# Kernel tuning notes

Hardware: AMD Instinct MI355X
Metric: run time of the kernel (lower is better)

The kernel has to match this reference:

```python
import jax, jax.numpy as jnp
import numpy as np
from jax import lax

BEV_SIZE = 250
BEV_RANGE = 50.0
BEV_RES = 0.4
SZ = BEV_SIZE * BEV_SIZE
N_POINTS = 5_000_000
EPS = 1e-5


def setup_inputs() -> dict:
    key = jax.random.key(0)
    ks = jax.random.split(key, 8)
    # points: x,y in [-55,55) (some out of range), z in [-3,5), intensity in [0,1)
    xy = jax.random.uniform(ks[0], (N_POINTS, 2), jnp.float32, -55.0, 55.0)
    z = jax.random.uniform(ks[1], (N_POINTS, 1), jnp.float32, -3.0, 5.0)
    it = jax.random.uniform(ks[2], (N_POINTS, 1), jnp.float32, 0.0, 1.0)
    points = jnp.concatenate([xy, z, it], axis=1)

    def he(k, shape):
        fan_in = shape[1] * shape[2] * shape[3]
        return jax.random.normal(k, shape, jnp.float32) * np.sqrt(2.0 / fan_in)

    return {
        "points": points,
        "w1": he(ks[3], (32, 4, 3, 3)), "b1": jnp.zeros(32), "g1": jnp.ones(32), "beta1": jnp.zeros(32),
        "w2": he(ks[4], (64, 32, 3, 3)), "b2": jnp.zeros(64), "g2": jnp.ones(64), "beta2": jnp.zeros(64),
        "w3": he(ks[5], (64, 64, 3, 3)), "b3": jnp.zeros(64), "g3": jnp.ones(64), "beta3": jnp.zeros(64),
    }


def points_to_bev(points):
    x, y, z, inten = points[:, 0], points[:, 1], points[:, 2], points[:, 3]
    valid = (x >= -BEV_RANGE) & (x < BEV_RANGE) & (y >= -BEV_RANGE) & (y < BEV_RANGE)
    xi = jnp.clip(((x + BEV_RANGE) / BEV_RES).astype(jnp.int32), 0, BEV_SIZE - 1)
    yi = jnp.clip(((y + BEV_RANGE) / BEV_RES).astype(jnp.int32), 0, BEV_SIZE - 1)
    # invalid points routed to an extra dummy bin SZ, sliced off afterwards
    flat = jnp.where(valid, yi * BEV_SIZE + xi, SZ)

    max_z = jnp.full(SZ + 1, -jnp.inf, jnp.float32).at[flat].max(z)[:SZ]
    max_z = jnp.where(jnp.isinf(max_z), 0.0, max_z)
    min_z = jnp.full(SZ + 1, jnp.inf, jnp.float32).at[flat].min(z)[:SZ]
    min_z = jnp.where(jnp.isinf(min_z), 0.0, min_z)
    density = jnp.zeros(SZ + 1, jnp.float32).at[flat].add(1.0)[:SZ]
    isum = jnp.zeros(SZ + 1, jnp.float32).at[flat].add(inten)[:SZ]
    mean_i = jnp.where(density > 0, isum / jnp.maximum(density, 1.0), 0.0)

    bev = jnp.stack([max_z, min_z, jnp.log1p(density), mean_i], axis=0)
    return bev.reshape(4, BEV_SIZE, BEV_SIZE)


def conv_bn_relu(x, w, b, g, beta):
    # x: (1, Cin, H, W), w: (Cout, Cin, 3, 3)
    y = lax.conv_general_dilated(x, w, (1, 1), "SAME",
                                 dimension_numbers=("NCHW", "OIHW", "NCHW"))
    y = y + b[None, :, None, None]
    # BatchNorm2d in training mode: batch stats over (N, H, W)
    mu = jnp.mean(y, axis=(0, 2, 3), keepdims=True)
    var = jnp.mean((y - mu) ** 2, axis=(0, 2, 3), keepdims=True)
    y = (y - mu) * lax.rsqrt(var + EPS)
    y = y * g[None, :, None, None] + beta[None, :, None, None]
    return jax.nn.relu(y)


def reference(points, w1, b1, g1, beta1, w2, b2, g2, beta2, w3, b3, g3, beta3):
    bev = points_to_bev(points)[None]  # (1, 4, 250, 250)
    h = conv_bn_relu(bev, w1, b1, g1, beta1)
    h = conv_bn_relu(h, w2, b2, g2, beta2)
    h = conv_bn_relu(h, w3, b3, g3, beta3)
    return h  # (1, 64, 250, 250)
```

## Files before the change

### kernel.cpp

```cpp
#include <hip/hip_runtime.h>


constexpr int BEVW = 250;
constexpr int SZC  = BEVW * BEVW;
constexpr int NB   = 512;
constexpr int PPT  = 16;
constexpr int CHUNK = 256 * PPT;
constexpr int NBKT = 100;
constexpr int NCELL = 625;
constexpr int CAPB = 43008;
constexpr int NSL  = 8;

__device__ __forceinline__ unsigned f2ord(float f) {
    unsigned u = __float_as_uint(f);
    return (u & 0x80000000u) ? ~u : (u | 0x80000000u);
}
__device__ __forceinline__ float ord2f(unsigned u) {
    unsigned b = (u & 0x80000000u) ? (u & 0x7FFFFFFFu) : ~u;
    return __uint_as_float(b);
}

__global__ void k_initg(unsigned* __restrict__ gcnt) {
    if (threadIdx.x < 128) gcnt[threadIdx.x] = 0u;
}

__launch_bounds__(256)
__global__ void k_bucket(const float4* __restrict__ pts, int n,
                         unsigned long long* __restrict__ recs,
                         unsigned* __restrict__ gcnt) {
    __shared__ unsigned lcnt[NBKT];
    __shared__ unsigned lbase[NBKT];
    const int tid = threadIdx.x;
    if (tid < NBKT) lcnt[tid] = 0u;
    __syncthreads();

    const int ppb = (n + NB - 1) / NB;
    const int start = blockIdx.x * ppb;
    const int end = min(start + ppb, n);

    for (int c0 = start; c0 < end; c0 += CHUNK) {
        unsigned long long rec[PPT];
        int bkt[PPT];
        unsigned slot[PPT];
        unsigned vmask = 0u;
#pragma unroll
        for (int k = 0; k < PPT; ++k) {
            int p = c0 + k * 256 + tid;
            if (p >= end) continue;
            float4 q = pts[p];
            if (!(q.x >= -50.0f && q.x < 50.0f && q.y >= -50.0f && q.y < 50.0f))
                continue;
            int xi = (int)((q.x + 50.0f) / 0.4f);
            int yi = (int)((q.y + 50.0f) / 0.4f);
            xi = min(max(xi, 0), BEVW - 1);
            yi = min(max(yi, 0), BEVW - 1);
            int b  = (yi / 25) * 10 + (xi / 25);
            int cl = (yi % 25) * 25 + (xi % 25);
            unsigned iq = (unsigned)(q.w * 4194304.0f);
            rec[k] = ((unsigned long long)f2ord(q.z) << 32) |
                     ((unsigned long long)(unsigned)cl << 22) | iq;
            bkt[k] = b;
            slot[k] = atomicAdd(&lcnt[b], 1u);
            vmask |= 1u << k;
        }
        __syncthreads();
        if (tid < NBKT) {
            unsigned c = lcnt[tid];
            if (c) lbase[tid] = atomicAdd(&gcnt[tid], c);
            lcnt[tid] = 0u;
        }
        __syncthreads();
#pragma unroll
        for (int k = 0; k < PPT; ++k) {
            if (!((vmask >> k) & 1u)) continue;
            unsigned idx = lbase[bkt[k]] + slot[k];
            if (idx < (unsigned)CAPB)
                recs[(size_t)bkt[k] * CAPB + idx] = rec[k];
        }
    }
}

__launch_bounds__(1024)
__global__ void k_reduce(const unsigned long long* __restrict__ recs,
                         const unsigned* __restrict__ gcnt,
                         float* __restrict__ bev) {
    __shared__ unsigned mxA[NCELL], mnA[NCELL], ctA[NCELL], siA[NCELL];
    const int b = blockIdx.x;
    for (int i = threadIdx.x; i < NCELL; i += 1024) {
        mxA[i] = 0u; mnA[i] = 0xFFFFFFFFu; ctA[i] = 0u; siA[i] = 0u;
    }
    __syncthreads();
    const unsigned nb = min(gcnt[b], (unsigned)CAPB);
    const unsigned long long* rb = recs + (size_t)b * CAPB;
    for (unsigned i = threadIdx.x; i < nb; i += 1024) {
        unsigned long long r = rb[i];
        unsigned zo = (unsigned)(r >> 32);
        unsigned cl = ((unsigned)(r >> 22)) & 0x3FFu;
        unsigned iq = (unsigned)r & 0x3FFFFFu;
        atomicMax(&mxA[cl], zo);
        atomicMin(&mnA[cl], zo);
        atomicAdd(&ctA[cl], 1u);
        atomicAdd(&siA[cl], iq);
    }
    __syncthreads();
    const int tx = b % 10, ty = b / 10;
    for (int i = threadIdx.x; i < NCELL; i += 1024) {
        int cy = ty * 25 + i / 25, cx = tx * 25 + i % 25;
        int cell = cy * BEVW + cx;
        unsigned c = ctA[i];
        bool has = c > 0u;
        float dn = (float)c;
        float isum = (float)siA[i] * (1.0f / 4194304.0f);
        bev[0 * SZC + cell] = has ? ord2f(mxA[i]) : 0.0f;
        bev[1 * SZC + cell] = has ? ord2f(mnA[i]) : 0.0f;
        bev[2 * SZC + cell] = log1pf(dn);
        bev[3 * SZC + cell] = has ? isum / dn : 0.0f;
    }
}

__global__ void k_wt(const float* __restrict__ w, float* __restrict__ wt,
                     int CIN, int COUT) {
    int i = blockIdx.x * blockDim.x + threadIdx.x;
    if (i >= COUT * CIN * 9) return;
    int oc = i / (CIN * 9);
    int r  = i % (CIN * 9);
    int ic = r / 9, k = r % 9;
    wt[(ic * 9 + k) * COUT + oc] = w[i];
}

template <int CIN, int COUT, int ICB, int OCG>
__launch_bounds__(256)
__global__ void k_conv3x3(const float* __restrict__ in, const float* __restrict__ wt,
                          const float* __restrict__ bias, float* __restrict__ out) {
    __shared__ float s_in[ICB][18][18];

    const int tid = threadIdx.x;
    const int px = tid & 15, py = tid >> 4;
    const int tile = blockIdx.x;
    const int tx = (tile & 15) * 16, ty = (tile >> 4) * 16;
    const int oc0 = blockIdx.y * OCG;

    float acc[OCG];
#pragma unroll
    for (int o = 0; o < OCG; ++o) acc[o] = 0.0f;

    for (int ic0 = 0; ic0 < CIN; ic0 += ICB) {
        __syncthreads();
        for (int e = tid; e < ICB * 18 * 18; e += 256) {
            int c = e / 324, r = (e % 324) / 18, q = e % 18;
            int gy = ty - 1 + r, gx = tx - 1 + q;
            float v = 0.0f;
            if (gy >= 0 && gy < BEVW && gx >= 0 && gx < BEVW)
                v = in[(ic0 + c) * SZC + gy * BEVW + gx];
            s_in[c][r][q] = v;
        }
        __syncthreads();

        for (int icl = 0; icl < ICB; ++icl) {
#pragma unroll
            for (int k = 0; k < 9; ++k) {
                float v = s_in[icl][py + k / 3][px + k % 3];
                const float* wk = wt + ((size_t)((ic0 + icl) * 9 + k) * COUT + oc0);
#pragma unroll
                for (int j = 0; j < OCG; ++j)
                    acc[j] = fmaf(v, wk[j], acc[j]);
            }
        }
    }

    int ox = tx + px, oy = ty + py;
    if (ox < BEVW && oy < BEVW) {
#pragma unroll
        for (int o = 0; o < OCG; ++o)
            out[(oc0 + o) * SZC + oy * BEVW + ox] = acc[o] + bias[oc0 + o];
    }
}

__global__ void k_bnstats1(const float* __restrict__ y, double* __restrict__ part) {
    const int c = blockIdx.x, s = blockIdx.y;
    const int lo = s * ((SZC + NSL - 1) / NSL);
    const int hi = min(lo + (SZC + NSL - 1) / NSL, SZC);
    const float* p = y + (size_t)c * SZC;
    double sm = 0.0, s2 = 0.0;
    for (int i = lo + threadIdx.x; i < hi; i += 256) {
        float v = p[i];
        sm += (double)v;
        s2 += (double)v * (double)v;
    }
    for (int off = 32; off; off >>= 1) {
        sm += __shfl_down(sm, off);
        s2 += __shfl_down(s2, off);
    }
    __shared__ double sh[8];
    int wid = threadIdx.x >> 6;
    if ((threadIdx.x & 63) == 0) { sh[wid * 2] = sm; sh[wid * 2 + 1] = s2; }
    __syncthreads();
    if (threadIdx.x == 0) {
        double S = 0.0, S2 = 0.0;
        for (int wv = 0; wv < 4; ++wv) { S += sh[wv * 2]; S2 += sh[wv * 2 + 1]; }
        part[(c * NSL + s) * 2]     = S;
        part[(c * NSL + s) * 2 + 1] = S2;
    }
}

__global__ void k_bnstats2(const double* __restrict__ part, float* __restrict__ stats) {
    int c = threadIdx.x;
    double S = 0.0, S2 = 0.0;
    for (int s = 0; s < NSL; ++s) {
        S  += part[(c * NSL + s) * 2];
        S2 += part[(c * NSL + s) * 2 + 1];
    }
    double mu  = S / (double)SZC;
    double var = S2 / (double)SZC - mu * mu;
    stats[c * 2]     = (float)mu;
    stats[c * 2 + 1] = (float)(1.0 / sqrt(var + 1e-5));
}

__global__ void k_bnrelu(const float* __restrict__ y, const float* __restrict__ stats,
                         const float* __restrict__ g, const float* __restrict__ beta,
                         float* __restrict__ out) {
    int c = blockIdx.y;
    int i = blockIdx.x * blockDim.x + threadIdx.x;
    if (i >= SZC) return;
    float mu = stats[c * 2], rs = stats[c * 2 + 1];
    size_t idx = (size_t)c * SZC + i;
    float v = (y[idx] - mu) * rs * g[c] + beta[c];
    out[idx] = v > 0.0f ? v : 0.0f;
}

extern "C" void kernel_launch(void* const* d_in, const int* in_sizes, int n_in,
                              void* d_out, int out_size, void* d_ws, size_t ws_size,
                              hipStream_t stream) {
    const float4* pts = (const float4*)d_in[0];
    const float* w1 = (const float*)d_in[1];
    const float* b1 = (const float*)d_in[2];
    const float* g1 = (const float*)d_in[3];
    const float* be1 = (const float*)d_in[4];
    const float* w2 = (const float*)d_in[5];
    const float* b2 = (const float*)d_in[6];
    const float* g2 = (const float*)d_in[7];
    const float* be2 = (const float*)d_in[8];
    const float* w3 = (const float*)d_in[9];
    const float* b3 = (const float*)d_in[10];
    const float* g3 = (const float*)d_in[11];
    const float* be3 = (const float*)d_in[12];

    float* ws = (float*)d_ws;
    unsigned long long* recs = (unsigned long long*)ws;
    constexpr size_t RECS_F = (size_t)NBKT * CAPB * 2;
    unsigned* gcnt = (unsigned*)(ws + RECS_F);
    float* bev = ws + RECS_F + 128;
    float* st1 = bev + 4 * SZC;
    float* st2 = st1 + 64;
    float* st3 = st2 + 128;
    double* bnpart = (double*)(st3 + 128);
    float* wt1 = (float*)(bnpart + 64 * NSL * 2);
    float* wt2 = wt1 + 32 * 4 * 9;
    float* wt3 = wt2 + 64 * 32 * 9;
    float* y1  = ws;
    float* y2  = ws + 2000000;
    float* out = (float*)d_out;

    int n = in_sizes[0] / 4;

    const int cellBlocks = (SZC + 255) / 256;

    k_wt<<<(32 * 4 * 9 + 255) / 256, 256, 0, stream>>>(w1, wt1, 4, 32);
    k_wt<<<(64 * 32 * 9 + 255) / 256, 256, 0, stream>>>(w2, wt2, 32, 64);
    k_wt<<<(64 * 64 * 9 + 255) / 256, 256, 0, stream>>>(w3, wt3, 64, 64);

    k_initg<<<1, 128, 0, stream>>>(gcnt);
    k_bucket<<<NB, 256, 0, stream>>>(pts, n, recs, gcnt);
    k_reduce<<<NBKT, 1024, 0, stream>>>(recs, gcnt, bev);

    k_conv3x3<4, 32, 4, 16><<<dim3(256, 2), 256, 0, stream>>>(bev, wt1, b1, y1);
    k_bnstats1<<<dim3(32, NSL), 256, 0, stream>>>(y1, bnpart);
    k_bnstats2<<<1, 32, 0, stream>>>(bnpart, st1);
    k_bnrelu<<<dim3(cellBlocks, 32), 256, 0, stream>>>(y1, st1, g1, be1, y1);

    k_conv3x3<32, 64, 8, 16><<<dim3(256, 4), 256, 0, stream>>>(y1, wt2, b2, y2);
    k_bnstats1<<<dim3(64, NSL), 256, 0, stream>>>(y2, bnpart);
    k_bnstats2<<<1, 64, 0, stream>>>(bnpart, st2);
    k_bnrelu<<<dim3(cellBlocks, 64), 256, 0, stream>>>(y2, st2, g2, be2, y2);

    k_conv3x3<64, 64, 8, 16><<<dim3(256, 4), 256, 0, stream>>>(y2, wt3, b3, out);
    k_bnstats1<<<dim3(64, NSL), 256, 0, stream>>>(out, bnpart);
    k_bnstats2<<<1, 64, 0, stream>>>(bnpart, st3);
    k_bnrelu<<<dim3(cellBlocks, 64), 256, 0, stream>>>(out, st3, g3, be3, out);
}
```

Measured before the change: 289.0 us.

## Fold BN+ReLU into next conv's input load and split-K conv over channels

The BatchNorm+ReLU of layers 1 and 2 is now applied while the next convolution loads its input tile, which removes two standalone elementwise passes over the activations. When the workspace is large enough, conv2 and conv3 split the input channels into two halves along grid z and write two partial outputs. Later kernels (stats, next conv, final BN+ReLU) sum those partials on read. The split doubles the grid to fill more CUs, at the cost of extra partial-buffer traffic and recomputing the BN affine in every halo load. The workspace layout moves to the tail of the buffer, and whether the split is used depends on ws_size.

```diff
diff --git a/kernel.cpp b/kernel.cpp
--- a/kernel.cpp
+++ b/kernel.cpp
@@ -128,10 +128,13 @@
     wt[(ic * 9 + k) * COUT + oc] = w[i];
 }
 
-template <int CIN, int COUT, int ICB, int OCG>
+template <int CINH, int COUT, int ICB, int OCG, bool FUSE_BN, bool SUM2, bool SPLIT>
 __launch_bounds__(256)
-__global__ void k_conv3x3(const float* __restrict__ in, const float* __restrict__ wt,
-                          const float* __restrict__ bias, float* __restrict__ out) {
+__global__ void k_conv(const float* __restrict__ ina, const float* __restrict__ inb,
+                       const float* __restrict__ wt, const float* __restrict__ bias,
+                       const float* __restrict__ stats, const float* __restrict__ g,
+                       const float* __restrict__ beta,
+                       float* __restrict__ outa, float* __restrict__ outb) {
     __shared__ float s_in[ICB][18][18];
 
     const int tid = threadIdx.x;
@@ -139,28 +142,40 @@
     const int tile = blockIdx.x;
     const int tx = (tile & 15) * 16, ty = (tile >> 4) * 16;
     const int oc0 = blockIdx.y * OCG;
+    const int z = SPLIT ? blockIdx.z : 0;
+    const int icB = z * CINH;
+    float* out = (SPLIT && z) ? outb : outa;
 
     float acc[OCG];
 #pragma unroll
     for (int o = 0; o < OCG; ++o) acc[o] = 0.0f;
 
-    for (int ic0 = 0; ic0 < CIN; ic0 += ICB) {
+    for (int ic0 = 0; ic0 < CINH; ic0 += ICB) {
         __syncthreads();
         for (int e = tid; e < ICB * 18 * 18; e += 256) {
             int c = e / 324, r = (e % 324) / 18, q = e % 18;
+            int cg = icB + ic0 + c;
             int gy = ty - 1 + r, gx = tx - 1 + q;
             float v = 0.0f;
-            if (gy >= 0 && gy < BEVW && gx >= 0 && gx < BEVW)
-                v = in[(ic0 + c) * SZC + gy * BEVW + gx];
+            if (gy >= 0 && gy < BEVW && gx >= 0 && gx < BEVW) {
+                size_t idx = (size_t)cg * SZC + gy * BEVW + gx;
+                v = ina[idx];
+                if (SUM2) v += inb[idx];
+                if (FUSE_BN) {
+                    float t = (v - stats[2 * cg]) * stats[2 * cg + 1] * g[cg] + beta[cg];
+                    v = t > 0.0f ? t : 0.0f;
+                }
+            }
             s_in[c][r][q] = v;
         }
         __syncthreads();
 
+#pragma unroll 2
         for (int icl = 0; icl < ICB; ++icl) {
 #pragma unroll
             for (int k = 0; k < 9; ++k) {
                 float v = s_in[icl][py + k / 3][px + k % 3];
-                const float* wk = wt + ((size_t)((ic0 + icl) * 9 + k) * COUT + oc0);
+                const float* wk = wt + ((size_t)((icB + ic0 + icl) * 9 + k) * COUT + oc0);
 #pragma unroll
                 for (int j = 0; j < OCG; ++j)
                     acc[j] = fmaf(v, wk[j], acc[j]);
@@ -170,20 +185,24 @@
 
     int ox = tx + px, oy = ty + py;
     if (ox < BEVW && oy < BEVW) {
+        const bool addb = (!SPLIT) || (z == 0);
 #pragma unroll
         for (int o = 0; o < OCG; ++o)
-            out[(oc0 + o) * SZC + oy * BEVW + ox] = acc[o] + bias[oc0 + o];
-    }
-}
-
-__global__ void k_bnstats1(const float* __restrict__ y, double* __restrict__ part) {
+            out[(oc0 + o) * SZC + oy * BEVW + ox] = acc[o] + (addb ? bias[oc0 + o] : 0.0f);
+    }
+}
+
+__global__ void k_bnstats1(const float* __restrict__ ya, const float* __restrict__ yb,
+                           double* __restrict__ part) {
     const int c = blockIdx.x, s = blockIdx.y;
     const int lo = s * ((SZC + NSL - 1) / NSL);
     const int hi = min(lo + (SZC + NSL - 1) / NSL, SZC);
-    const float* p = y + (size_t)c * SZC;
+    const float* pa = ya + (size_t)c * SZC;
+    const float* pb = yb ? yb + (size_t)c * SZC : nullptr;
     double sm = 0.0, s2 = 0.0;
     for (int i = lo + threadIdx.x; i < hi; i += 256) {
-        float v = p[i];
+        float v = pa[i];
+        if (pb) v += pb[i];
         sm += (double)v;
         s2 += (double)v * (double)v;
     }
@@ -216,15 +235,17 @@
     stats[c * 2 + 1] = (float)(1.0 / sqrt(var + 1e-5));
 }
 
-__global__ void k_bnrelu(const float* __restrict__ y, const float* __restrict__ stats,
-                         const float* __restrict__ g, const float* __restrict__ beta,
-                         float* __restrict__ out) {
+__global__ void k_bnreluS(const float* __restrict__ ya, const float* __restrict__ yb,
+                          const float* __restrict__ stats, const float* __restrict__ g,
+                          const float* __restrict__ beta, float* __restrict__ out) {
     int c = blockIdx.y;
     int i = blockIdx.x * blockDim.x + threadIdx.x;
     if (i >= SZC) return;
     float mu = stats[c * 2], rs = stats[c * 2 + 1];
     size_t idx = (size_t)c * SZC + i;
-    float v = (y[idx] - mu) * rs * g[c] + beta[c];
+    float v = ya[idx];
+    if (yb) v += yb[idx];
+    v = (v - mu) * rs * g[c] + beta[c];
     out[idx] = v > 0.0f ? v : 0.0f;
 }
 
@@ -246,23 +267,32 @@
     const float* be3 = (const float*)d_in[12];
 
     float* ws = (float*)d_ws;
-    unsigned long long* recs = (unsigned long long*)ws;
-    constexpr size_t RECS_F = (size_t)NBKT * CAPB * 2;
-    unsigned* gcnt = (unsigned*)(ws + RECS_F);
-    float* bev = ws + RECS_F + 128;
+    const size_t wsf = ws_size / 4;
+
+    constexpr size_t TAILF = 128 + 250000 + 64 + 128 + 128 + 2048 + 1152 + 18432 + 36864;
+    float* tail = ws + (wsf - TAILF);
+    unsigned* gcnt = (unsigned*)tail;
+    float* bev = tail + 128;
     float* st1 = bev + 4 * SZC;
     float* st2 = st1 + 64;
     float* st3 = st2 + 128;
-    double* bnpart = (double*)(st3 + 128);
-    float* wt1 = (float*)(bnpart + 64 * NSL * 2);
-    float* wt2 = wt1 + 32 * 4 * 9;
-    float* wt3 = wt2 + 64 * 32 * 9;
+    float* pst = st3 + 128;
+    double* bnpart = (double*)pst;
+    float* wt1 = pst + 2048;
+    float* wt2 = wt1 + 1152;
+    float* wt3 = wt2 + 18432;
+
+    const size_t tailF = wsf - TAILF;
+    unsigned long long* recs = (unsigned long long*)ws;
     float* y1  = ws;
-    float* y2  = ws + 2000000;
-    float* out = (float*)d_out;
+    float* y2a = ws + 2000000;
+    const bool split2 = tailF >= 14000000ULL;
+    const bool split3 = tailF >= 10000000ULL;
+    float* y2b  = split2 ? ws + 6000000 : nullptr;
+    float* outb = split3 ? (split2 ? ws + 10000000 : ws + 6000000) : nullptr;
+    float* outa = (float*)d_out;
 
     int n = in_sizes[0] / 4;
-
     const int cellBlocks = (SZC + 255) / 256;
 
     k_wt<<<(32 * 4 * 9 + 255) / 256, 256, 0, stream>>>(w1, wt1, 4, 32);
@@ -273,18 +303,40 @@
     k_bucket<<<NB, 256, 0, stream>>>(pts, n, recs, gcnt);
     k_reduce<<<NBKT, 1024, 0, stream>>>(recs, gcnt, bev);
 
-    k_conv3x3<4, 32, 4, 16><<<dim3(256, 2), 256, 0, stream>>>(bev, wt1, b1, y1);
-    k_bnstats1<<<dim3(32, NSL), 256, 0, stream>>>(y1, bnpart);
+    k_conv<4, 32, 4, 16, false, false, false>
+        <<<dim3(256, 2, 1), 256, 0, stream>>>(bev, nullptr, wt1, b1,
+                                              nullptr, nullptr, nullptr, y1, nullptr);
+    k_bnstats1<<<dim3(32, NSL), 256, 0, stream>>>(y1, nullptr, bnpart);
     k_bnstats2<<<1, 32, 0, stream>>>(bnpart, st1);
-    k_bnrelu<<<dim3(cellBlocks, 32), 256, 0, stream>>>(y1, st1, g1, be1, y1);
-
-    k_conv3x3<32, 64, 8, 16><<<dim3(256, 4), 256, 0, stream>>>(y1, wt2, b2, y2);
-    k_bnstats1<<<dim3(64, NSL), 256, 0, stream>>>(y2, bnpart);
+
+    if (split2)
+        k_conv<16, 64, 8, 16, true, false, true>
+            <<<dim3(256, 4, 2), 256, 0, stream>>>(y1, nullptr, wt2, b2,
+                                                  st1, g1, be1, y2a, y2b);
+    else
+        k_conv<32, 64, 8, 16, true, false, false>
+            <<<dim3(256, 4, 1), 256, 0, stream>>>(y1, nullptr, wt2, b2,
+                                                  st1, g1, be1, y2a, nullptr);
+    k_bnstats1<<<dim3(64, NSL), 256, 0, stream>>>(y2a, y2b, bnpart);
     k_bnstats2<<<1, 64, 0, stream>>>(bnpart, st2);
-    k_bnrelu<<<dim3(cellBlocks, 64), 256, 0, stream>>>(y2, st2, g2, be2, y2);
-
-    k_conv3x3<64, 64, 8, 16><<<dim3(256, 4), 256, 0, stream>>>(y2, wt3, b3, out);
-    k_bnstats1<<<dim3(64, NSL), 256, 0, stream>>>(out, bnpart);
+
+    if (split3) {
+        if (split2)
+            k_conv<32, 64, 8, 16, true, true, true>
+                <<<dim3(256, 4, 2), 256, 0, stream>>>(y2a, y2b, wt3, b3,
+                                                      st2, g2, be2, outa, outb);
+        else
+            k_conv<32, 64, 8, 16, true, false, true>
+                <<<dim3(256, 4, 2), 256, 0, stream>>>(y2a, nullptr, wt3, b3,
+                                                      st2, g2, be2, outa, outb);
+    } else {
+        k_conv<64, 64, 8, 16, true, false, false>
+            <<<dim3(256, 4, 1), 256, 0, stream>>>(y2a, nullptr, wt3, b3,
+                                                  st2, g2, be2, outa, nullptr);
+    }
+    k_bnstats1<<<dim3(64, NSL), 256, 0, stream>>>(outa, outb, bnpart);
     k_bnstats2<<<1, 64, 0, stream>>>(bnpart, st3);
-    k_bnrelu<<<dim3(cellBlocks, 64), 256, 0, stream>>>(out, st3, g3, be3, out);
-}
+
+    k_bnreluS<<<dim3(cellBlocks, 64), 256, 0, stream>>>(outa, outb, st3, g3, be3,
+                                                        (float*)d_out);
+}
```

Measured after the change: 333.3 us. 15.4% more time.

## Fuse BN stats into conv epilogue and BN-ReLU into next conv load

Applied to the files above, without the earlier changes.

Each conv block now computes per-tile partial sums and sums of squares in its epilogue, so the separate BN statistics passes are gone. BN scale/shift is folded into one (A,B) pair per channel and applied with ReLU while the next conv loads its input, which removes the intermediate bn-relu passes. The conv itself moves to 32x32 tiles with 2x2 outputs per thread and double-buffered shared-memory staging of 4 input channels. The cost is far fewer blocks (256 per layer) and higher register pressure, which may leave the GPU underoccupied.

```diff
diff --git a/kernel.cpp b/kernel.cpp
--- a/kernel.cpp
+++ b/kernel.cpp
@@ -9,7 +9,7 @@
 constexpr int NBKT = 100;
 constexpr int NCELL = 625;
 constexpr int CAPB = 43008;
-constexpr int NSL  = 8;
+constexpr int NTILE = 64;
 
 __device__ __forceinline__ unsigned f2ord(float f) {
     unsigned u = __float_as_uint(f);
@@ -128,104 +128,171 @@
     wt[(ic * 9 + k) * COUT + oc] = w[i];
 }
 
-template <int CIN, int COUT, int ICB, int OCG>
+template <int CIN, int COUT, int OCG, bool FUSE>
 __launch_bounds__(256)
-__global__ void k_conv3x3(const float* __restrict__ in, const float* __restrict__ wt,
-                          const float* __restrict__ bias, float* __restrict__ out) {
-    __shared__ float s_in[ICB][18][18];
+__global__ void k_conv(const float* __restrict__ in, const float* __restrict__ wt,
+                       const float* __restrict__ bias, const float* __restrict__ ab,
+                       float* __restrict__ out, double* __restrict__ bnpart) {
+    constexpr int ICB = 4;
+    constexpr int PH  = CIN / ICB;
+    constexpr int TW  = 34;
+    constexpr int TE  = ICB * TW * TW;
+    constexpr int NJ  = (TE + 255) / 256;
+    __shared__ float s_in[2][ICB][TW * TW];
+    __shared__ double s_red[4][OCG][2];
 
     const int tid = threadIdx.x;
-    const int px = tid & 15, py = tid >> 4;
+    const int u = tid & 15, v = tid >> 4;
     const int tile = blockIdx.x;
-    const int tx = (tile & 15) * 16, ty = (tile >> 4) * 16;
+    const int tx = (tile & 7) * 32, ty = (tile >> 3) * 32;
     const int oc0 = blockIdx.y * OCG;
-
-    float acc[OCG];
-#pragma unroll
-    for (int o = 0; o < OCG; ++o) acc[o] = 0.0f;
-
-    for (int ic0 = 0; ic0 < CIN; ic0 += ICB) {
+    const int lane = tid & 63, wid = tid >> 6;
+
+    float acc[2][2][OCG];
+#pragma unroll
+    for (int a = 0; a < 2; ++a)
+#pragma unroll
+        for (int b = 0; b < 2; ++b)
+#pragma unroll
+            for (int o = 0; o < OCG; ++o) acc[a][b][o] = 0.0f;
+
+#pragma unroll
+    for (int j = 0; j < NJ; ++j) {
+        int e = j * 256 + tid;
+        if (e < TE) {
+            int c = e / (TW * TW), rem = e % (TW * TW);
+            int r = rem / TW, q = rem % TW;
+            int gy = ty - 1 + r, gx = tx - 1 + q;
+            float x = 0.0f;
+            if (gy >= 0 && gy < BEVW && gx >= 0 && gx < BEVW) {
+                x = in[(size_t)c * SZC + gy * BEVW + gx];
+                if (FUSE) x = fmaxf(fmaf(x, ab[2 * c], ab[2 * c + 1]), 0.0f);
+            }
+            s_in[0][c][rem] = x;
+        }
+    }
+    __syncthreads();
+
+#pragma unroll 1
+    for (int t = 0; t < PH; ++t) {
+        const int cur = t & 1;
+        float rv[NJ];
+        if (t + 1 < PH) {
+            const int icn = (t + 1) * ICB;
+#pragma unroll
+            for (int j = 0; j < NJ; ++j) {
+                int e = j * 256 + tid;
+                rv[j] = 0.0f;
+                if (e < TE) {
+                    int c = e / (TW * TW), rem = e % (TW * TW);
+                    int r = rem / TW, q = rem % TW;
+                    int gy = ty - 1 + r, gx = tx - 1 + q;
+                    if (gy >= 0 && gy < BEVW && gx >= 0 && gx < BEVW) {
+                        int cg = icn + c;
+                        float x = in[(size_t)cg * SZC + gy * BEVW + gx];
+                        if (FUSE) x = fmaxf(fmaf(x, ab[2 * cg], ab[2 * cg + 1]), 0.0f);
+                        rv[j] = x;
+                    }
+                }
+            }
+        }
+
+#pragma unroll
+        for (int icl = 0; icl < ICB; ++icl) {
+            const float* sp = &s_in[cur][icl][0];
+            float vv[4][4];
+#pragma unroll
+            for (int rr = 0; rr < 4; ++rr) {
+                float2 a = *(const float2*)(sp + (2 * v + rr) * TW + 2 * u);
+                float2 b = *(const float2*)(sp + (2 * v + rr) * TW + 2 * u + 2);
+                vv[rr][0] = a.x; vv[rr][1] = a.y; vv[rr][2] = b.x; vv[rr][3] = b.y;
+            }
+            const int icg = t * ICB + icl;
+#pragma unroll
+            for (int tap = 0; tap < 9; ++tap) {
+                const int ky = tap / 3, kx = tap % 3;
+                const float* wk = wt + ((size_t)(icg * 9 + tap) * COUT + oc0);
+#pragma unroll
+                for (int o = 0; o < OCG; ++o) {
+                    float w = wk[o];
+                    acc[0][0][o] = fmaf(vv[ky][kx],         w, acc[0][0][o]);
+                    acc[0][1][o] = fmaf(vv[ky][kx + 1],     w, acc[0][1][o]);
+                    acc[1][0][o] = fmaf(vv[ky + 1][kx],     w, acc[1][0][o]);
+                    acc[1][1][o] = fmaf(vv[ky + 1][kx + 1], w, acc[1][1][o]);
+                }
+            }
+        }
+
+        if (t + 1 < PH) {
+#pragma unroll
+            for (int j = 0; j < NJ; ++j) {
+                int e = j * 256 + tid;
+                if (e < TE) s_in[cur ^ 1][e / (TW * TW)][e % (TW * TW)] = rv[j];
+            }
+        }
         __syncthreads();
-        for (int e = tid; e < ICB * 18 * 18; e += 256) {
-            int c = e / 324, r = (e % 324) / 18, q = e % 18;
-            int gy = ty - 1 + r, gx = tx - 1 + q;
-            float v = 0.0f;
-            if (gy >= 0 && gy < BEVW && gx >= 0 && gx < BEVW)
-                v = in[(ic0 + c) * SZC + gy * BEVW + gx];
-            s_in[c][r][q] = v;
-        }
-        __syncthreads();
-
-        for (int icl = 0; icl < ICB; ++icl) {
-#pragma unroll
-            for (int k = 0; k < 9; ++k) {
-                float v = s_in[icl][py + k / 3][px + k % 3];
-                const float* wk = wt + ((size_t)((ic0 + icl) * 9 + k) * COUT + oc0);
-#pragma unroll
-                for (int j = 0; j < OCG; ++j)
-                    acc[j] = fmaf(v, wk[j], acc[j]);
-            }
-        }
-    }
-
-    int ox = tx + px, oy = ty + py;
-    if (ox < BEVW && oy < BEVW) {
-#pragma unroll
-        for (int o = 0; o < OCG; ++o)
-            out[(oc0 + o) * SZC + oy * BEVW + ox] = acc[o] + bias[oc0 + o];
-    }
-}
-
-__global__ void k_bnstats1(const float* __restrict__ y, double* __restrict__ part) {
-    const int c = blockIdx.x, s = blockIdx.y;
-    const int lo = s * ((SZC + NSL - 1) / NSL);
-    const int hi = min(lo + (SZC + NSL - 1) / NSL, SZC);
-    const float* p = y + (size_t)c * SZC;
-    double sm = 0.0, s2 = 0.0;
-    for (int i = lo + threadIdx.x; i < hi; i += 256) {
-        float v = p[i];
-        sm += (double)v;
-        s2 += (double)v * (double)v;
-    }
-    for (int off = 32; off; off >>= 1) {
-        sm += __shfl_down(sm, off);
-        s2 += __shfl_down(s2, off);
-    }
-    __shared__ double sh[8];
-    int wid = threadIdx.x >> 6;
-    if ((threadIdx.x & 63) == 0) { sh[wid * 2] = sm; sh[wid * 2 + 1] = s2; }
-    __syncthreads();
-    if (threadIdx.x == 0) {
+    }
+
+    const int ox = tx + 2 * u, oy = ty + 2 * v;
+    const bool vx = ox < BEVW;
+    const bool vy0 = oy < BEVW, vy1 = (oy + 1) < BEVW;
+#pragma unroll
+    for (int o = 0; o < OCG; ++o) {
+        float bs = bias[oc0 + o];
+        float y00 = acc[0][0][o] + bs, y01 = acc[0][1][o] + bs;
+        float y10 = acc[1][0][o] + bs, y11 = acc[1][1][o] + bs;
+        if (vx && vy0)
+            *(float2*)&out[(size_t)(oc0 + o) * SZC + oy * BEVW + ox] = make_float2(y00, y01);
+        if (vx && vy1)
+            *(float2*)&out[(size_t)(oc0 + o) * SZC + (oy + 1) * BEVW + ox] = make_float2(y10, y11);
+        double s = 0.0, s2 = 0.0;
+        if (vx && vy0) {
+            s += (double)y00 + (double)y01;
+            s2 += (double)y00 * y00 + (double)y01 * y01;
+        }
+        if (vx && vy1) {
+            s += (double)y10 + (double)y11;
+            s2 += (double)y10 * y10 + (double)y11 * y11;
+        }
+#pragma unroll
+        for (int off = 32; off; off >>= 1) {
+            s  += __shfl_down(s, off);
+            s2 += __shfl_down(s2, off);
+        }
+        if (lane == 0) { s_red[wid][o][0] = s; s_red[wid][o][1] = s2; }
+    }
+    __syncthreads();
+    if (tid < OCG) {
         double S = 0.0, S2 = 0.0;
-        for (int wv = 0; wv < 4; ++wv) { S += sh[wv * 2]; S2 += sh[wv * 2 + 1]; }
-        part[(c * NSL + s) * 2]     = S;
-        part[(c * NSL + s) * 2 + 1] = S2;
-    }
-}
-
-__global__ void k_bnstats2(const double* __restrict__ part, float* __restrict__ stats) {
+#pragma unroll
+        for (int wv = 0; wv < 4; ++wv) { S += s_red[wv][tid][0]; S2 += s_red[wv][tid][1]; }
+        bnpart[((size_t)(oc0 + tid) * NTILE + tile) * 2]     = S;
+        bnpart[((size_t)(oc0 + tid) * NTILE + tile) * 2 + 1] = S2;
+    }
+}
+
+__global__ void k_bnstats2(const double* __restrict__ part, const float* __restrict__ g,
+                           const float* __restrict__ beta, float* __restrict__ statsAB) {
     int c = threadIdx.x;
     double S = 0.0, S2 = 0.0;
-    for (int s = 0; s < NSL; ++s) {
-        S  += part[(c * NSL + s) * 2];
-        S2 += part[(c * NSL + s) * 2 + 1];
+    for (int t = 0; t < NTILE; ++t) {
+        S  += part[((size_t)c * NTILE + t) * 2];
+        S2 += part[((size_t)c * NTILE + t) * 2 + 1];
     }
     double mu  = S / (double)SZC;
     double var = S2 / (double)SZC - mu * mu;
-    stats[c * 2]     = (float)mu;
-    stats[c * 2 + 1] = (float)(1.0 / sqrt(var + 1e-5));
-}
-
-__global__ void k_bnrelu(const float* __restrict__ y, const float* __restrict__ stats,
-                         const float* __restrict__ g, const float* __restrict__ beta,
-                         float* __restrict__ out) {
+    double A = (1.0 / sqrt(var + 1e-5)) * (double)g[c];
+    statsAB[2 * c]     = (float)A;
+    statsAB[2 * c + 1] = (float)((double)beta[c] - mu * A);
+}
+
+__global__ void k_bnreluS(const float* __restrict__ y, const float* __restrict__ ab,
+                          float* __restrict__ out) {
     int c = blockIdx.y;
     int i = blockIdx.x * blockDim.x + threadIdx.x;
     if (i >= SZC) return;
-    float mu = stats[c * 2], rs = stats[c * 2 + 1];
     size_t idx = (size_t)c * SZC + i;
-    float v = (y[idx] - mu) * rs * g[c] + beta[c];
-    out[idx] = v > 0.0f ? v : 0.0f;
+    out[idx] = fmaxf(fmaf(y[idx], ab[2 * c], ab[2 * c + 1]), 0.0f);
 }
 
 extern "C" void kernel_launch(void* const* d_in, const int* in_sizes, int n_in,
@@ -246,23 +313,26 @@
     const float* be3 = (const float*)d_in[12];
 
     float* ws = (float*)d_ws;
-    unsigned long long* recs = (unsigned long long*)ws;
-    constexpr size_t RECS_F = (size_t)NBKT * CAPB * 2;
-    unsigned* gcnt = (unsigned*)(ws + RECS_F);
-    float* bev = ws + RECS_F + 128;
+    const size_t wsf = ws_size / 4;
+
+    constexpr size_t TAILF = 128 + 250000 + 64 + 128 + 128 + 16384 + 1152 + 18432 + 36864;
+    float* tail = ws + (wsf - TAILF);
+    unsigned* gcnt = (unsigned*)tail;
+    float* bev = tail + 128;
     float* st1 = bev + 4 * SZC;
     float* st2 = st1 + 64;
     float* st3 = st2 + 128;
     double* bnpart = (double*)(st3 + 128);
-    float* wt1 = (float*)(bnpart + 64 * NSL * 2);
-    float* wt2 = wt1 + 32 * 4 * 9;
-    float* wt3 = wt2 + 64 * 32 * 9;
-    float* y1  = ws;
-    float* y2  = ws + 2000000;
+    float* wt1 = st3 + 128 + 16384;
+    float* wt2 = wt1 + 1152;
+    float* wt3 = wt2 + 18432;
+
+    unsigned long long* recs = (unsigned long long*)ws;
+    float* y1 = ws;
+    float* y2 = ws + 2000000;
     float* out = (float*)d_out;
 
     int n = in_sizes[0] / 4;
-
     const int cellBlocks = (SZC + 255) / 256;
 
     k_wt<<<(32 * 4 * 9 + 255) / 256, 256, 0, stream>>>(w1, wt1, 4, 32);
@@ -273,18 +343,14 @@
     k_bucket<<<NB, 256, 0, stream>>>(pts, n, recs, gcnt);
     k_reduce<<<NBKT, 1024, 0, stream>>>(recs, gcnt, bev);
 
-    k_conv3x3<4, 32, 4, 16><<<dim3(256, 2), 256, 0, stream>>>(bev, wt1, b1, y1);
-    k_bnstats1<<<dim3(32, NSL), 256, 0, stream>>>(y1, bnpart);
-    k_bnstats2<<<1, 32, 0, stream>>>(bnpart, st1);
-    k_bnrelu<<<dim3(cellBlocks, 32), 256, 0, stream>>>(y1, st1, g1, be1, y1);
-
-    k_conv3x3<32, 64, 8, 16><<<dim3(256, 4), 256, 0, stream>>>(y1, wt2, b2, y2);
-    k_bnstats1<<<dim3(64, NSL), 256, 0, stream>>>(y2, bnpart);
-    k_bnstats2<<<1, 64, 0, stream>>>(bnpart, st2);
-    k_bnrelu<<<dim3(cellBlocks, 64), 256, 0, stream>>>(y2, st2, g2, be2, y2);
-
-    k_conv3x3<64, 64, 8, 16><<<dim3(256, 4), 256, 0, stream>>>(y2, wt3, b3, out);
-    k_bnstats1<<<dim3(64, NSL), 256, 0, stream>>>(out, bnpart);
-    k_bnstats2<<<1, 64, 0, stream>>>(bnpart, st3);
-    k_bnrelu<<<dim3(cellBlocks, 64), 256, 0, stream>>>(out, st3, g3, be3, out);
-}
+    k_conv<4, 32, 16, false><<<dim3(NTILE, 2), 256, 0, stream>>>(bev, wt1, b1, nullptr, y1, bnpart);
+    k_bnstats2<<<1, 32, 0, stream>>>(bnpart, g1, be1, st1);
+
+    k_conv<32, 64, 16, true><<<dim3(NTILE, 4), 256, 0, stream>>>(y1, wt2, b2, st1, y2, bnpart);
+    k_bnstats2<<<1, 64, 0, stream>>>(bnpart, g2, be2, st2);
+
+    k_conv<64, 64, 16, true><<<dim3(NTILE, 4), 256, 0, stream>>>(y2, wt3, b3, st2, out, bnpart);
+    k_bnstats2<<<1, 64, 0, stream>>>(bnpart, g3, be3, st3);
+
+    k_bnreluS<<<dim3(cellBlocks, 64), 256, 0, stream>>>(out, st3, out);
+}
```

Measured after the change: 623.2 us. 116% more time.
